# Kernel optimization log

Hardware: AMD Instinct MI355X
Metric: run time of the kernel (lower is better)

The kernel has to match this reference:

```python
import jax, jax.numpy as jnp
import numpy as np
from jax import lax

TEMPERATURE = 0.5
MOMENTUM = 0.9
EPS = 1e-12  # F.normalize eps

B, D, K = 8192, 512, 16384


def _l2norm(x):
    # matches F.normalize(p=2): x / max(||x||, eps)
    n = jnp.sqrt(jnp.sum(x * x, axis=-1, keepdims=True))
    return x / jnp.maximum(n, EPS)


def setup_inputs() -> dict:
    key = jax.random.key(0)
    k1, k2, k3 = jax.random.split(key, 3)
    embeddings = jax.random.normal(k1, (B, D), dtype=jnp.float32)
    cluster_ids = jax.random.randint(k2, (B,), 0, K, dtype=jnp.int64)
    prototypes = jax.random.normal(k3, (K, D), dtype=jnp.float32)
    return {"embeddings": embeddings, "cluster_ids": cluster_ids, "prototypes": prototypes}


def reference(embeddings, cluster_ids, prototypes):
    emb_n = _l2norm(embeddings)            # [B, D]
    proto_n = _l2norm(prototypes)          # [K, D]
    sim = jnp.einsum('bd,kd->bk', emb_n, proto_n) / TEMPERATURE  # [B, K]

    pos = jnp.take_along_axis(sim, cluster_ids[:, None], axis=1)  # [B, 1]
    # mask out the positive column, then stable logsumexp over negatives
    is_pos = jnp.arange(sim.shape[1])[None, :] == cluster_ids[:, None]  # [B, K]
    neg = jnp.where(is_pos, -jnp.inf, sim)
    lse = jax.scipy.special.logsumexp(neg, axis=1, keepdims=True)       # [B, 1]
    loss = jnp.mean(-pos + lse)

    # serial momentum EMA update (order-dependent for duplicate cluster ids)
    def step(protos, xc):
        x, c = xc
        row = MOMENTUM * protos[c] + (1.0 - MOMENTUM) * x
        return protos.at[c].set(row), None

    new_protos, _ = lax.scan(step, prototypes, (embeddings, cluster_ids))
    return loss, new_protos
```

## Files before the change

### kernel.cpp

```cpp
#include <hip/hip_runtime.h>
#include <hip/hip_bf16.h>


#define B_N 8192
#define D_N 512
#define K_N 16384
#define INV_T 2.0f
#define MOM 0.9f

#define BM 128
#define KSPLIT 8
#define NSTEP 64
#define BUFB 16384
#define CAP 64

typedef __attribute__((ext_vector_type(8))) int intx8;
typedef __attribute__((ext_vector_type(4))) float floatx4;

__device__ __forceinline__ void gl_lds16(const void* g, void* lds) {
    __builtin_amdgcn_global_load_lds(
        (const __attribute__((address_space(1))) void*)g,
        (__attribute__((address_space(3))) void*)lds, 16, 0, 0);
}

__device__ __forceinline__ intx8 frag2(const unsigned char* rp, int o0, int o1) {
    intx8 v;
    ((int4*)&v)[0] = *(const int4*)(rp + o0);
    ((int4*)&v)[1] = *(const int4*)(rp + o1);
    return v;
}

__device__ __forceinline__ floatx4 mxfma(intx8 a, intx8 b, floatx4 c) {
    return __builtin_amdgcn_mfma_scale_f32_16x16x128_f8f6f4(a, b, c, 0, 0, 0,
                                                            0x7F7F7F7F, 0, 0x7F7F7F7F);
}

__global__ void norm_kernel(const float* __restrict__ emb, const float* __restrict__ pro,
                            unsigned char* __restrict__ embq, unsigned char* __restrict__ proq,
                            float* __restrict__ rowsum, float* __restrict__ out) {
    if (blockIdx.x < 32) rowsum[blockIdx.x * 256 + threadIdx.x] = 0.0f;
    if (blockIdx.x == 32 && threadIdx.x == 0) out[0] = 0.0f;
    int row = blockIdx.x * 4 + (threadIdx.x >> 6);
    int lane = threadIdx.x & 63;
    const float* x;
    unsigned char* o;
    if (row < B_N) {
        x = emb + (size_t)row * D_N;
        o = embq + (size_t)row * D_N;
    } else {
        x = pro + (size_t)(row - B_N) * D_N;
        o = proq + (size_t)(row - B_N) * D_N;
    }
    const float4* xp = (const float4*)(x + lane * 8);
    float4 v0 = xp[0];
    float4 v1 = xp[1];
    float ss = v0.x * v0.x + v0.y * v0.y + v0.z * v0.z + v0.w * v0.w +
               v1.x * v1.x + v1.y * v1.y + v1.z * v1.z + v1.w * v1.w;
    #pragma unroll
    for (int of = 32; of; of >>= 1) ss += __shfl_xor(ss, of);
    float sc = 16.0f / fmaxf(sqrtf(ss), 1e-12f);
    int w0 = 0, w1 = 0;
    w0 = __builtin_amdgcn_cvt_pk_fp8_f32(v0.x * sc, v0.y * sc, w0, false);
    w0 = __builtin_amdgcn_cvt_pk_fp8_f32(v0.z * sc, v0.w * sc, w0, true);
    w1 = __builtin_amdgcn_cvt_pk_fp8_f32(v1.x * sc, v1.y * sc, w1, false);
    w1 = __builtin_amdgcn_cvt_pk_fp8_f32(v1.z * sc, v1.w * sc, w1, true);
    int2 st = {w0, w1};
    *(int2*)(o + lane * 8) = st;
}

__global__ void pos_kernel(const float* __restrict__ emb, const float* __restrict__ pro,
                           const int* __restrict__ cid, float* __restrict__ rowpos) {
    int b = blockIdx.x * 4 + (threadIdx.x >> 6);
    int lane = threadIdx.x & 63;
    int c = cid[b];
    const float4* ep = (const float4*)(emb + (size_t)b * D_N + lane * 8);
    const float4* pp = (const float4*)(pro + (size_t)c * D_N + lane * 8);
    float4 e0 = ep[0], e1 = ep[1], p0 = pp[0], p1 = pp[1];
    float dp = e0.x * p0.x + e0.y * p0.y + e0.z * p0.z + e0.w * p0.w +
               e1.x * p1.x + e1.y * p1.y + e1.z * p1.z + e1.w * p1.w;
    float ee = e0.x * e0.x + e0.y * e0.y + e0.z * e0.z + e0.w * e0.w +
               e1.x * e1.x + e1.y * e1.y + e1.z * e1.z + e1.w * e1.w;
    float qq = p0.x * p0.x + p0.y * p0.y + p0.z * p0.z + p0.w * p0.w +
               p1.x * p1.x + p1.y * p1.y + p1.z * p1.z + p1.w * p1.w;
    #pragma unroll
    for (int o = 32; o; o >>= 1) {
        dp += __shfl_xor(dp, o);
        ee += __shfl_xor(ee, o);
        qq += __shfl_xor(qq, o);
    }
    if (lane == 0)
        rowpos[b] = INV_T * dp / (fmaxf(sqrtf(ee), 1e-12f) * fmaxf(sqrtf(qq), 1e-12f));
}

__global__ __launch_bounds__(256, 4) void flash_kernel(const unsigned char* __restrict__ embq,
                                                       const unsigned char* __restrict__ proq,
                                                       float* __restrict__ rowsum_g) {
    __shared__ __align__(16) unsigned char Bs[2 * BUFB];
    const int t = threadIdx.x;
    const int w = t >> 6, lane = t & 63;
    const int quad = lane >> 4, lcol = lane & 15;

    const int wgl = blockIdx.x;
    const int ks = wgl & 7;
    const int rowBase = (wgl >> 3) * BM;
    const int kb = ks * (K_N / KSPLIT);

    const int fsw0 = (((quad << 1) | 0) ^ (lcol & 7)) << 4;
    const int fsw1 = (((quad << 1) | 1) ^ (lcol & 7)) << 4;

    const int srow = w * 2 + (lane >> 5);
    const int g = lane & 31;
    const unsigned char* bS = proq + (size_t)(kb + srow) * D_N + ((g >> 3) << 7) +
                              (((g & 7) ^ (srow & 7)) << 4);

    float rs[8];
    #pragma unroll
    for (int i = 0; i < 8; i++) rs[i] = 0.0f;

    intx8 afr[4][2];
    {
        const unsigned char* aBase =
            embq + (size_t)(rowBase + w * 32 + lcol) * D_N + quad * 32;
        #pragma unroll
        for (int ch = 0; ch < 4; ch++)
            #pragma unroll
            for (int mi = 0; mi < 2; mi++) {
                const unsigned char* p = aBase + (size_t)mi * (16 * D_N) + (ch << 7);
                ((int4*)&afr[ch][mi])[0] = *(const int4*)(p);
                ((int4*)&afr[ch][mi])[1] = *(const int4*)(p + 16);
            }
    }
    #pragma unroll
    for (int p = 0; p < 4; p++)
        gl_lds16(bS + (size_t)p * 8 * D_N, Bs + p * 4096 + w * 1024);
    __syncthreads();

    const unsigned char* bSrc = bS + (size_t)32 * D_N;
    for (int s = 0; s < NSTEP; s++) {
        if (s + 1 < NSTEP) {
            unsigned char* d = Bs + ((s + 1) & 1) * BUFB + w * 1024;
            #pragma unroll
            for (int p = 0; p < 4; p++)
                gl_lds16(bSrc + (size_t)p * 8 * D_N, d + p * 4096);
        }
        bSrc += (size_t)32 * D_N;

        const unsigned char* rb0 = Bs + (s & 1) * BUFB + lcol * 512;
        const unsigned char* rb1 = rb0 + 16 * 512;
        floatx4 a00 = {0.f, 0.f, 0.f, 0.f}, a01 = {0.f, 0.f, 0.f, 0.f};
        floatx4 a10 = {0.f, 0.f, 0.f, 0.f}, a11 = {0.f, 0.f, 0.f, 0.f};
        __builtin_amdgcn_s_setprio(1);
        #pragma unroll
        for (int ch = 0; ch < 4; ch++) {
            intx8 b0 = frag2(rb0 + (ch << 7), fsw0, fsw1);
            intx8 b1 = frag2(rb1 + (ch << 7), fsw0, fsw1);
            a00 = mxfma(afr[ch][0], b0, a00);
            a01 = mxfma(afr[ch][0], b1, a01);
            a10 = mxfma(afr[ch][1], b0, a10);
            a11 = mxfma(afr[ch][1], b1, a11);
        }
        __builtin_amdgcn_s_setprio(0);

        #pragma unroll
        for (int r = 0; r < 4; r++) {
            rs[r] += __expf(a00[r] * (INV_T / 256.0f)) + __expf(a01[r] * (INV_T / 256.0f));
            rs[4 + r] += __expf(a10[r] * (INV_T / 256.0f)) + __expf(a11[r] * (INV_T / 256.0f));
        }

        __syncthreads();
    }

    #pragma unroll
    for (int i = 0; i < 8; i++) {
        #pragma unroll
        for (int o = 1; o < 16; o <<= 1) rs[i] += __shfl_xor(rs[i], o);
    }
    if (lcol == 0) {
        #pragma unroll
        for (int mi = 0; mi < 2; mi++)
            #pragma unroll
            for (int r = 0; r < 4; r++)
                atomicAdd(&rowsum_g[rowBase + w * 32 + mi * 16 + quad * 4 + r],
                          rs[mi * 4 + r]);
    }
}

__global__ void loss_kernel(const float* __restrict__ rowsum, const float* __restrict__ rowpos,
                            float* __restrict__ out, int* __restrict__ cnt) {
    __shared__ float red[256];
    int t = threadIdx.x;
    int b = blockIdx.x * 256 + t;
    cnt[b * 2] = 0;
    cnt[b * 2 + 1] = 0;
    float p = rowpos[b];
    red[t] = logf(rowsum[b] - __expf(p)) - p;
    __syncthreads();
    for (int o = 128; o; o >>= 1) {
        if (t < o) red[t] += red[t + o];
        __syncthreads();
    }
    if (t == 0) atomicAdd(out, red[0] * (1.0f / (float)B_N));
}

__global__ void ema_count(const int* __restrict__ cid, int* __restrict__ cnt,
                          int* __restrict__ bucket) {
    int b = blockIdx.x * 256 + threadIdx.x;
    int c = cid[b];
    int slot = atomicAdd(&cnt[c], 1);
    if (slot < CAP) bucket[c * CAP + slot] = b;
}

__global__ void ema_apply(const float* __restrict__ emb, const float* __restrict__ pro,
                          const int* __restrict__ cnt, const int* __restrict__ bucket,
                          float* __restrict__ outp) {
    int k = blockIdx.x * 4 + (threadIdx.x >> 6);
    int lane = threadIdx.x & 63;
    int n = cnt[k];
    n = n < CAP ? n : CAP;
    const float4* pp = (const float4*)(pro + (size_t)k * D_N + lane * 8);
    float4 a0 = pp[0], a1 = pp[1];
    int myb = (lane < n) ? bucket[k * CAP + lane] : 0x7fffffff;
    for (int i = 0; i < n; i++) {
        int m = myb;
        #pragma unroll
        for (int o = 1; o < 64; o <<= 1) {
            int v = __shfl_xor(m, o);
            m = v < m ? v : m;
        }
        const float4* ep = (const float4*)(emb + (size_t)m * D_N + lane * 8);
        float4 e0 = ep[0], e1 = ep[1];
        a0.x = MOM * a0.x + (1.0f - MOM) * e0.x;
        a0.y = MOM * a0.y + (1.0f - MOM) * e0.y;
        a0.z = MOM * a0.z + (1.0f - MOM) * e0.z;
        a0.w = MOM * a0.w + (1.0f - MOM) * e0.w;
        a1.x = MOM * a1.x + (1.0f - MOM) * e1.x;
        a1.y = MOM * a1.y + (1.0f - MOM) * e1.y;
        a1.z = MOM * a1.z + (1.0f - MOM) * e1.z;
        a1.w = MOM * a1.w + (1.0f - MOM) * e1.w;
        if (myb == m) myb = 0x7fffffff;
    }
    float4* op = (float4*)(outp + (size_t)k * D_N + lane * 8);
    op[0] = a0;
    op[1] = a1;
}

extern "C" void kernel_launch(void* const* d_in, const int* in_sizes, int n_in,
                              void* d_out, int out_size, void* d_ws, size_t ws_size,
                              hipStream_t stream) {
    const float* emb = (const float*)d_in[0];
    const int* cid = (const int*)d_in[1];
    const float* pro = (const float*)d_in[2];
    float* out = (float*)d_out;

    char* ws = (char*)d_ws;
    unsigned char* embq = (unsigned char*)ws;
    unsigned char* proq = (unsigned char*)(ws + 4194304);
    float* rowsum = (float*)(ws + 12582912);
    float* rowpos = (float*)(ws + 12615680);
    int* cnt = (int*)(ws + 4194304);
    int* bucket = (int*)(ws + 4194304 + 65536);

    norm_kernel<<<(B_N + K_N) / 4, 256, 0, stream>>>(emb, pro, embq, proq, rowsum, out);
    pos_kernel<<<B_N / 4, 256, 0, stream>>>(emb, pro, cid, rowpos);
    flash_kernel<<<dim3(64 * KSPLIT), 256, 0, stream>>>(embq, proq, rowsum);
    loss_kernel<<<B_N / 256, 256, 0, stream>>>(rowsum, rowpos, out, cnt);
    ema_count<<<B_N / 256, 256, 0, stream>>>(cid, cnt, bucket);
    ema_apply<<<K_N / 4, 256, 0, stream>>>(emb, pro, cnt, bucket, out + 1);
}
```

Before: 198.4 us.

## Stream prototype fragments directly into registers instead of staging through LDS

The flash kernel drops the LDS double buffer, the async global-to-LDS copies and the per-step block barrier. Each wave now loads its own prototype MFMA fragments straight from global memory into a register ping-pong buffer. Each wave now covers 64 embedding rows instead of 32, and KSPLIT rises from 8 to 16, which halves the column range per block and keeps the grid at 512 blocks. Removing the barriers and LDS round-trips trades against loading each prototype tile once per wave instead of once per block, which doubles L2 read traffic. Higher register use and launch bounds of 2 may also leave less latency hiding.

```diff
diff --git a/kernel.cpp b/kernel.cpp
--- a/kernel.cpp
+++ b/kernel.cpp
@@ -8,27 +8,12 @@
 #define INV_T 2.0f
 #define MOM 0.9f
 
-#define BM 128
-#define KSPLIT 8
+#define KSPLIT 16
 #define NSTEP 64
-#define BUFB 16384
 #define CAP 64
 
 typedef __attribute__((ext_vector_type(8))) int intx8;
 typedef __attribute__((ext_vector_type(4))) float floatx4;
-
-__device__ __forceinline__ void gl_lds16(const void* g, void* lds) {
-    __builtin_amdgcn_global_load_lds(
-        (const __attribute__((address_space(1))) void*)g,
-        (__attribute__((address_space(3))) void*)lds, 16, 0, 0);
-}
-
-__device__ __forceinline__ intx8 frag2(const unsigned char* rp, int o0, int o1) {
-    intx8 v;
-    ((int4*)&v)[0] = *(const int4*)(rp + o0);
-    ((int4*)&v)[1] = *(const int4*)(rp + o1);
-    return v;
-}
 
 __device__ __forceinline__ floatx4 mxfma(intx8 a, intx8 b, floatx4 c) {
     return __builtin_amdgcn_mfma_scale_f32_16x16x128_f8f6f4(a, b, c, 0, 0, 0,
@@ -92,96 +77,89 @@
         rowpos[b] = INV_T * dp / (fmaxf(sqrtf(ee), 1e-12f) * fmaxf(sqrtf(qq), 1e-12f));
 }
 
-__global__ __launch_bounds__(256, 4) void flash_kernel(const unsigned char* __restrict__ embq,
+#define LOADB(BUF, S)                                                                 \
+    do {                                                                              \
+        const unsigned char* _q = bBase + (size_t)(S) * (16 * D_N);                   \
+        _Pragma("unroll")                                                             \
+        for (int ch = 0; ch < 4; ch++) {                                              \
+            ((int4*)&BUF[ch])[0] = *(const int4*)(_q + (ch << 7));                    \
+            ((int4*)&BUF[ch])[1] = *(const int4*)(_q + (ch << 7) + 16);               \
+        }                                                                             \
+    } while (0)
+
+#define PHASE(BUF)                                                                    \
+    do {                                                                              \
+        floatx4 a0 = {0.f, 0.f, 0.f, 0.f}, a1 = {0.f, 0.f, 0.f, 0.f};                \
+        floatx4 a2 = {0.f, 0.f, 0.f, 0.f}, a3 = {0.f, 0.f, 0.f, 0.f};                \
+        __builtin_amdgcn_s_setprio(1);                                                \
+        _Pragma("unroll")                                                             \
+        for (int ch = 0; ch < 4; ch++) {                                              \
+            a0 = mxfma(afr[ch][0], BUF[ch], a0);                                      \
+            a1 = mxfma(afr[ch][1], BUF[ch], a1);                                      \
+            a2 = mxfma(afr[ch][2], BUF[ch], a2);                                      \
+            a3 = mxfma(afr[ch][3], BUF[ch], a3);                                      \
+        }                                                                             \
+        __builtin_amdgcn_s_setprio(0);                                                \
+        _Pragma("unroll")                                                             \
+        for (int r = 0; r < 4; r++) {                                                 \
+            rs[r] += __expf(a0[r] * (INV_T / 256.0f));                                \
+            rs[4 + r] += __expf(a1[r] * (INV_T / 256.0f));                            \
+            rs[8 + r] += __expf(a2[r] * (INV_T / 256.0f));                            \
+            rs[12 + r] += __expf(a3[r] * (INV_T / 256.0f));                           \
+        }                                                                             \
+    } while (0)
+
+__global__ __launch_bounds__(256, 2) void flash_kernel(const unsigned char* __restrict__ embq,
                                                        const unsigned char* __restrict__ proq,
                                                        float* __restrict__ rowsum_g) {
-    __shared__ __align__(16) unsigned char Bs[2 * BUFB];
     const int t = threadIdx.x;
     const int w = t >> 6, lane = t & 63;
     const int quad = lane >> 4, lcol = lane & 15;
 
-    const int wgl = blockIdx.x;
-    const int ks = wgl & 7;
-    const int rowBase = (wgl >> 3) * BM;
+    const int ks = blockIdx.x & 15;
+    const int band = blockIdx.x >> 4;
+    const int rowBase = band * 256 + w * 64;
     const int kb = ks * (K_N / KSPLIT);
 
-    const int fsw0 = (((quad << 1) | 0) ^ (lcol & 7)) << 4;
-    const int fsw1 = (((quad << 1) | 1) ^ (lcol & 7)) << 4;
-
-    const int srow = w * 2 + (lane >> 5);
-    const int g = lane & 31;
-    const unsigned char* bS = proq + (size_t)(kb + srow) * D_N + ((g >> 3) << 7) +
-                              (((g & 7) ^ (srow & 7)) << 4);
-
-    float rs[8];
-    #pragma unroll
-    for (int i = 0; i < 8; i++) rs[i] = 0.0f;
-
-    intx8 afr[4][2];
+    intx8 afr[4][4];
     {
-        const unsigned char* aBase =
-            embq + (size_t)(rowBase + w * 32 + lcol) * D_N + quad * 32;
+        const unsigned char* aBase = embq + (size_t)(rowBase + lcol) * D_N + quad * 32;
         #pragma unroll
         for (int ch = 0; ch < 4; ch++)
             #pragma unroll
-            for (int mi = 0; mi < 2; mi++) {
+            for (int mi = 0; mi < 4; mi++) {
                 const unsigned char* p = aBase + (size_t)mi * (16 * D_N) + (ch << 7);
                 ((int4*)&afr[ch][mi])[0] = *(const int4*)(p);
                 ((int4*)&afr[ch][mi])[1] = *(const int4*)(p + 16);
             }
     }
-    #pragma unroll
-    for (int p = 0; p < 4; p++)
-        gl_lds16(bS + (size_t)p * 8 * D_N, Bs + p * 4096 + w * 1024);
-    __syncthreads();
-
-    const unsigned char* bSrc = bS + (size_t)32 * D_N;
-    for (int s = 0; s < NSTEP; s++) {
-        if (s + 1 < NSTEP) {
-            unsigned char* d = Bs + ((s + 1) & 1) * BUFB + w * 1024;
-            #pragma unroll
-            for (int p = 0; p < 4; p++)
-                gl_lds16(bSrc + (size_t)p * 8 * D_N, d + p * 4096);
-        }
-        bSrc += (size_t)32 * D_N;
-
-        const unsigned char* rb0 = Bs + (s & 1) * BUFB + lcol * 512;
-        const unsigned char* rb1 = rb0 + 16 * 512;
-        floatx4 a00 = {0.f, 0.f, 0.f, 0.f}, a01 = {0.f, 0.f, 0.f, 0.f};
-        floatx4 a10 = {0.f, 0.f, 0.f, 0.f}, a11 = {0.f, 0.f, 0.f, 0.f};
-        __builtin_amdgcn_s_setprio(1);
-        #pragma unroll
-        for (int ch = 0; ch < 4; ch++) {
-            intx8 b0 = frag2(rb0 + (ch << 7), fsw0, fsw1);
-            intx8 b1 = frag2(rb1 + (ch << 7), fsw0, fsw1);
-            a00 = mxfma(afr[ch][0], b0, a00);
-            a01 = mxfma(afr[ch][0], b1, a01);
-            a10 = mxfma(afr[ch][1], b0, a10);
-            a11 = mxfma(afr[ch][1], b1, a11);
-        }
-        __builtin_amdgcn_s_setprio(0);
-
-        #pragma unroll
-        for (int r = 0; r < 4; r++) {
-            rs[r] += __expf(a00[r] * (INV_T / 256.0f)) + __expf(a01[r] * (INV_T / 256.0f));
-            rs[4 + r] += __expf(a10[r] * (INV_T / 256.0f)) + __expf(a11[r] * (INV_T / 256.0f));
-        }
-
-        __syncthreads();
-    }
-
-    #pragma unroll
-    for (int i = 0; i < 8; i++) {
+
+    const unsigned char* bBase = proq + (size_t)(kb + lcol) * D_N + quad * 32;
+
+    float rs[16];
+    #pragma unroll
+    for (int i = 0; i < 16; i++) rs[i] = 0.0f;
+
+    intx8 bfA[4], bfB[4];
+    LOADB(bfA, 0);
+    for (int s = 0; s < NSTEP; s += 2) {
+        if (s + 1 < NSTEP) LOADB(bfB, s + 1);
+        PHASE(bfA);
+        if (s + 2 < NSTEP) LOADB(bfA, s + 2);
+        PHASE(bfB);
+    }
+
+    #pragma unroll
+    for (int i = 0; i < 16; i++) {
         #pragma unroll
         for (int o = 1; o < 16; o <<= 1) rs[i] += __shfl_xor(rs[i], o);
     }
     if (lcol == 0) {
         #pragma unroll
-        for (int mi = 0; mi < 2; mi++)
+        for (int mi = 0; mi < 4; mi++)
             #pragma unroll
             for (int r = 0; r < 4; r++)
-                atomicAdd(&rowsum_g[rowBase + w * 32 + mi * 16 + quad * 4 + r],
-                          rs[mi * 4 + r]);
+                atomicAdd(&rowsum_g[rowBase + mi * 16 + quad * 4 + r], rs[mi * 4 + r]);
     }
 }
 
@@ -262,7 +240,7 @@
 
     norm_kernel<<<(B_N + K_N) / 4, 256, 0, stream>>>(emb, pro, embq, proq, rowsum, out);
     pos_kernel<<<B_N / 4, 256, 0, stream>>>(emb, pro, cid, rowpos);
-    flash_kernel<<<dim3(64 * KSPLIT), 256, 0, stream>>>(embq, proq, rowsum);
+    flash_kernel<<<dim3(32 * KSPLIT), 256, 0, stream>>>(embq, proq, rowsum);
     loss_kernel<<<B_N / 256, 256, 0, stream>>>(rowsum, rowpos, out, cnt);
     ema_count<<<B_N / 256, 256, 0, stream>>>(cid, cnt, bucket);
     ema_apply<<<K_N / 4, 256, 0, stream>>>(emb, pro, cnt, bucket, out + 1);
```

Measured after the change: 260.7 us. 31.4% more time.
